# Kernel optimization log

Measured on AMD Instinct MI355X. Metric: run time of the kernel, lower is better.

The kernel has to match this reference:

```python
import jax, jax.numpy as jnp
import numpy as np

B, T, S = 64, 48, 48
E, H, L, V = 512, 1024, 2, 32000


def setup_inputs() -> dict:
    key = jax.random.key(0)
    ks = jax.random.split(key, 16)
    s = 0.02
    return {
        "tgt_input": jax.random.randint(ks[0], (B, T), 0, V),
        "h0": jax.random.normal(ks[1], (L, B, H), jnp.float32),
        "c0": jax.random.normal(ks[2], (L, B, H), jnp.float32),
        "encoder_output": jax.random.normal(ks[3], (B, S, H), jnp.float32),
        "src_key_padding_mask": jnp.zeros((B, S), bool),
        "embedding": jax.random.normal(ks[4], (V, E), jnp.float32) * s,
        "W_l": jax.random.normal(ks[5], (H, H), jnp.float32) * s,
        "b_l": jnp.zeros((H,), jnp.float32),
        "W_ih0": jax.random.normal(ks[6], (4 * H, E + H), jnp.float32) * s,
        "W_hh0": jax.random.normal(ks[7], (4 * H, H), jnp.float32) * s,
        "b_ih0": jnp.zeros((4 * H,), jnp.float32),
        "b_hh0": jnp.zeros((4 * H,), jnp.float32),
        "W_ih1": jax.random.normal(ks[8], (4 * H, H), jnp.float32) * s,
        "W_hh1": jax.random.normal(ks[9], (4 * H, H), jnp.float32) * s,
        "b_ih1": jnp.zeros((4 * H,), jnp.float32),
        "b_hh1": jnp.zeros((4 * H,), jnp.float32),
    }


def _lstm_cell(x, h, c, W_ih, W_hh, b_ih, b_hh):
    # PyTorch gate order: i, f, g, o
    gates = x @ W_ih.T + b_ih + h @ W_hh.T + b_hh  # [B, 4H]
    i, f, g, o = jnp.split(gates, 4, axis=-1)
    c_new = jax.nn.sigmoid(f) * c + jax.nn.sigmoid(i) * jnp.tanh(g)
    h_new = jax.nn.sigmoid(o) * jnp.tanh(c_new)
    return h_new, c_new


def reference(tgt_input, h0, c0, encoder_output, src_key_padding_mask,
              embedding, W_l, b_l,
              W_ih0, W_hh0, b_ih0, b_hh0,
              W_ih1, W_hh1, b_ih1, b_hh1):
    emb = embedding[tgt_input]              # [B, T, E]
    emb_t = jnp.transpose(emb, (1, 0, 2))   # [T, B, E]
    layers = ((W_ih0, W_hh0, b_ih0, b_hh0), (W_ih1, W_hh1, b_ih1, b_hh1))

    def step(carry, x_t):
        h, c = carry                        # [L, B, H] each
        # Luong attention with query = last-layer hidden state
        q = h[-1] @ W_l.T + b_l             # [B, H]
        scores = jnp.einsum('bh,bsh->bs', q, encoder_output)
        scores = jnp.where(src_key_padding_mask, -jnp.inf, scores)
        attn = jax.nn.softmax(scores, axis=-1)
        ctx = jnp.einsum('bs,bsh->bh', attn, encoder_output)  # [B, H]
        x = jnp.concatenate([x_t, ctx], axis=-1)              # [B, E+H]
        new_h, new_c = [], []
        for l, (W_ih, W_hh, b_ih, b_hh) in enumerate(layers):
            hn, cn = _lstm_cell(x, h[l], c[l], W_ih, W_hh, b_ih, b_hh)
            new_h.append(hn)
            new_c.append(cn)
            x = hn
        return (jnp.stack(new_h), jnp.stack(new_c)), x  # x = top-layer output

    (hn, cn), outs = jax.lax.scan(step, (h0, c0), emb_t)
    outputs = jnp.transpose(outs, (1, 0, 2))  # [B, T, H]
    return outputs, hn, cn
```

## Files before the change

kernel.cpp:

```cpp
#include <hip/hip_runtime.h>
#include <stdint.h>


using short8 = __attribute__((ext_vector_type(8))) short;
using f32x4  = __attribute__((ext_vector_type(4))) float;
typedef unsigned short u16;
typedef unsigned long long u64;

#define B_  64
#define T_  48
#define S_  48
#define H_  1024
#define E_  512

__device__ __forceinline__ float bf2f(u16 u) {
    union { unsigned int i; float f; } v; v.i = ((unsigned int)u) << 16; return v.f;
}
__device__ __forceinline__ u16 f2bf(float f) {
    union { float f; unsigned int i; } v; v.f = f;
    unsigned int r = v.i + 0x7fff + ((v.i >> 16) & 1);
    return (u16)(r >> 16);
}
__device__ __forceinline__ float sigm(float x) { return 1.f / (1.f + __expf(-x)); }


__global__ void cast_copy(u16* __restrict__ dst, int dld, int doff,
                          const float* __restrict__ src, int sld, int soff,
                          int rows, int colshift) {
    int cols = 1 << colshift;
    int total = rows << colshift;
    for (int i = blockIdx.x * blockDim.x + threadIdx.x; i < total;
         i += gridDim.x * blockDim.x) {
        int r = i >> colshift, c = i & (cols - 1);
        dst[(size_t)r * dld + doff + c] = f2bf(src[(size_t)r * sld + soff + c]);
    }
}

__global__ void transpose_cast(u16* __restrict__ dst, const float* __restrict__ src) {
    int idx = blockIdx.x * blockDim.x + threadIdx.x;
    int r = idx >> 10, c = idx & 1023;
    dst[idx] = f2bf(src[(size_t)c * 1024 + r]);
}

__global__ void embed_gather(u16* __restrict__ embA, const float* __restrict__ emb,
                             const int* __restrict__ tgt) {
    int row = blockIdx.x;
    int t = row >> 6, b = row & 63;
    int id = tgt[b * T_ + t];
    const float* s = emb + (size_t)id * E_;
    u16* d = embA + (size_t)row * E_;
    for (int e = threadIdx.x; e < E_; e += blockDim.x) d[e] = f2bf(s[e]);
}

__global__ void sbias_kernel(float* __restrict__ sbias, const float* __restrict__ enc,
                             const float* __restrict__ b_l) {
    int r = blockIdx.x, lane = threadIdx.x;
    const float* e = enc + (size_t)r * H_;
    float acc = 0.f;
    for (int k = lane; k < H_; k += 64) acc += b_l[k] * e[k];
    for (int o = 32; o; o >>= 1) acc += __shfl_xor(acc, o);
    if (lane == 0) sbias[r] = acc;
}

__global__ void init_state(u16* __restrict__ xa0_0, u16* __restrict__ xa1_0,
                           const float* __restrict__ h0) {
    int i = blockIdx.x * blockDim.x + threadIdx.x;
    int l = i >> 16, rem = i & 65535, b = rem >> 10, c = rem & 1023;
    u16 hb = f2bf(h0[i]);
    if (l == 0) xa0_0[b * 2048 + 1024 + c] = hb;
    else        xa1_0[b * 2048 + 1024 + c] = hb;
}

__global__ __launch_bounds__(256) void gemm64(
    const u16* __restrict__ A, const u16* __restrict__ W, u16* __restrict__ D,
    const float* __restrict__ bias1, const float* __restrict__ bias2,
    int N, int Kd)
{
    __shared__ float part[4][64][65];
    int tid = threadIdx.x, w = tid >> 6, lane = tid & 63;
    int hf = lane >> 4, q = lane & 15;
    int n0 = blockIdx.x * 64, m0 = blockIdx.y * 64;
    int ks = Kd >> 2;
    int kb = w * ks + hf * 8;
    const u16* ap = A + (size_t)(m0 + q) * Kd + kb;
    const u16* wp = W + (size_t)(n0 + q) * Kd + kb;
    f32x4 acc[4][4] = {};
    for (int k0 = 0; k0 < ks; k0 += 32) {
        short8 bf[4], af[4];
#pragma unroll
        for (int n = 0; n < 4; ++n) bf[n] = *(const short8*)(wp + (size_t)n * 16 * Kd + k0);
#pragma unroll
        for (int m = 0; m < 4; ++m) af[m] = *(const short8*)(ap + (size_t)m * 16 * Kd + k0);
#pragma unroll
        for (int m = 0; m < 4; ++m)
#pragma unroll
            for (int n = 0; n < 4; ++n)
                acc[m][n] = __builtin_amdgcn_mfma_f32_16x16x32_bf16(af[m], bf[n], acc[m][n], 0, 0, 0);
    }
#pragma unroll
    for (int m = 0; m < 4; ++m)
#pragma unroll
        for (int n = 0; n < 4; ++n)
#pragma unroll
            for (int r = 0; r < 4; ++r)
                part[w][m * 16 + hf * 4 + r][n * 16 + q] = acc[m][n][r];
    __syncthreads();
#pragma unroll
    for (int k = 0; k < 16; ++k) {
        int o = tid + k * 256;
        int row = o >> 6, col = o & 63;
        float v = part[0][row][col] + part[1][row][col]
                + part[2][row][col] + part[3][row][col];
        if (bias1) v += bias1[n0 + col] + bias2[n0 + col];
        D[(size_t)(m0 + row) * N + n0 + col] = f2bf(v);
    }
}


struct PParams {
    const float *W_ih0, *W_hh0, *W_ih1, *W_hh1;
    const u16  *preG, *encW, *encB;
    const float *sbias, *b_ih1, *b_hh1, *c0in;
    const unsigned char* mask;
    u16 *XA0, *XA1;
    float *out, *hn0, *hn1, *cn0, *cn1;
    unsigned *cnt;
};

__device__ __forceinline__ void gridarrive(unsigned* cnt, int ep, int g) {
    __syncthreads();
    if (threadIdx.x == 0)
        __hip_atomic_fetch_add(&cnt[g * 256 + ep], 1u,
                               __ATOMIC_RELAXED, __HIP_MEMORY_SCOPE_AGENT);
    asm volatile("" ::: "memory");
}
__device__ __forceinline__ void gridpoll(unsigned* cnt, int ep) {
    if (threadIdx.x < 64) {
        int spin = 0;
        for (;;) {
            unsigned v = __hip_atomic_load(&cnt[threadIdx.x * 256 + ep],
                                           __ATOMIC_RELAXED,
                                           __HIP_MEMORY_SCOPE_AGENT);
            if (__ballot(v >= 4u) == ~0ull) break;
            __builtin_amdgcn_s_sleep(2);
            if (++spin > (1 << 20)) break;
        }
    }
    asm volatile("" ::: "memory");
    __syncthreads();
}

__global__ void __launch_bounds__(256, 1) decoder_persistent(PParams P) {
    __shared__ u16 wlds[2][4096][8];
    __shared__ union {
        struct { float h1f[1056]; float sc[48][4]; float pr[48]; } at;
        float gates[64][20];
    } sm;

    const int tid = threadIdx.x, blk = blockIdx.x;
    const int w = tid >> 6, lane = tid & 63, g4 = lane >> 4, q = lane & 15;
    const int b2 = tid >> 2, j2 = tid & 3;
    const int colg = blk * 4 + j2;

    {
        int r = tid & 15, cb = tid >> 4;
        int grow = (r >> 2) * 1024 + blk * 4 + (r & 3);
#pragma unroll
        for (int l = 0; l < 2; ++l) {
            const float* Sa = l ? P.W_ih1 : P.W_ih0;
            const float* Sb = l ? P.W_hh1 : P.W_hh0;
            int sld  = l ? 1024 : 1536;
            int soff = l ? 0 : 512;
            for (int it = 0; it < 16; ++it) {
                int c = cb + it * 16;
                int k = c * 8;
                const float* src = (k < 1024)
                    ? (Sa + (size_t)grow * sld + soff + k)
                    : (Sb + (size_t)grow * 1024 + (k - 1024));
                float4 x0 = *(const float4*)(src);
                float4 x1 = *(const float4*)(src + 4);
                short8 v;
                v[0] = f2bf(x0.x); v[1] = f2bf(x0.y); v[2] = f2bf(x0.z); v[3] = f2bf(x0.w);
                v[4] = f2bf(x1.x); v[5] = f2bf(x1.y); v[6] = f2bf(x1.z); v[7] = f2bf(x1.w);
                *(short8*)&wlds[l][c * 16 + r][0] = v;
            }
        }
    }
    __syncthreads();
    float bsum[4];
#pragma unroll
    for (int g = 0; g < 4; ++g)
        bsum[g] = P.b_ih1[g * 1024 + colg] + P.b_hh1[g * 1024 + colg];
    float c0r = P.c0in[b2 * 1024 + colg];
    float c1r = P.c0in[65536 + b2 * 1024 + colg];

    const int ab = (blk & 7) * 8 + ((blk >> 3) & 7);
    const int aq = blk >> 6;
    int ep = 0;
    int t = 0;

    auto gemm_half = [&](const u16* Abase, int layer, int kbase, f32x4 seed) -> f32x4 {
        const u16* ap = Abase + (size_t)(w * 16 + q) * 2048 + kbase + g4 * 8;
        short8 xa[32];
#pragma unroll
        for (int kk = 0; kk < 32; ++kk)
            xa[kk] = *(const short8*)(ap + kk * 32);
        f32x4 a0 = seed, a1 = {}, a2 = {}, a3 = {};
        const int cbs = (kbase >> 3) + g4;
#pragma unroll
        for (int kk = 0; kk < 32; kk += 4) {
            a0 = __builtin_amdgcn_mfma_f32_16x16x32_bf16(
                xa[kk + 0], *(const short8*)&wlds[layer][(cbs + (kk + 0) * 4) * 16 + q][0], a0, 0, 0, 0);
            a1 = __builtin_amdgcn_mfma_f32_16x16x32_bf16(
                xa[kk + 1], *(const short8*)&wlds[layer][(cbs + (kk + 1) * 4) * 16 + q][0], a1, 0, 0, 0);
            a2 = __builtin_amdgcn_mfma_f32_16x16x32_bf16(
                xa[kk + 2], *(const short8*)&wlds[layer][(cbs + (kk + 2) * 4) * 16 + q][0], a2, 0, 0, 0);
            a3 = __builtin_amdgcn_mfma_f32_16x16x32_bf16(
                xa[kk + 3], *(const short8*)&wlds[layer][(cbs + (kk + 3) * 4) * 16 + q][0], a3, 0, 0, 0);
        }
        return (a0 + a1) + (a2 + a3);
    };

    auto lstm_phase = [&](const u16* Abase, int layer, f32x4 seed,
                          float add0, float add1, float add2, float add3,
                          float& creg, u16* dA, u16* dB, float* outp,
                          float* hnO, float* cnO, int doLast) {
        f32x4 g = gemm_half(Abase, layer, 0, seed);
#pragma unroll
        for (int r = 0; r < 4; ++r) sm.gates[w * 16 + g4 * 4 + r][q] = g[r];
        __syncthreads();
        float gi = sm.gates[b2][j2]      + add0;
        float gf = sm.gates[b2][4 + j2]  + add1;
        float gg = sm.gates[b2][8 + j2]  + add2;
        float go = sm.gates[b2][12 + j2] + add3;
        float cnew = sigm(gf) * creg + sigm(gi) * tanhf(gg);
        float hnew = sigm(go) * tanhf(cnew);
        creg = cnew;
        ((u16*)&sm.gates[b2][16])[j2] = f2bf(hnew);
        if (outp) outp[(size_t)(b2 * T_ + t) * H_ + colg] = hnew;
        if (doLast) { hnO[b2 * 1024 + colg] = hnew; cnO[b2 * 1024 + colg] = cnew; }
        __syncthreads();
        if (tid < 64) {
            u64 pk;
            __builtin_memcpy(&pk, (const u16*)&sm.gates[tid][16], 8);
            __hip_atomic_store((u64*)(dA + tid * 2048 + blk * 4), pk,
                               __ATOMIC_RELAXED, __HIP_MEMORY_SCOPE_AGENT);
            if (dB)
                __hip_atomic_store((u64*)(dB + tid * 2048 + blk * 4), pk,
                                   __ATOMIC_RELAXED, __HIP_MEMORY_SCOPE_AGENT);
        }
    };

    for (t = 0; t < T_; ++t) {
        const int last = (t == T_ - 1);
        u16* xa0c = P.XA0 + (size_t)t * 131072;
        u16* xa0n = P.XA0 + (size_t)(t + 1) * 131072;
        u16* xa1c = P.XA1 + (size_t)t * 131072;
        u16* xa1n = P.XA1 + (size_t)(t + 1) * 131072;

        for (int i = tid; i < H_; i += 256)
            sm.at.h1f[(i >> 8) * 264 + (i & 255)] = bf2f(xa1c[ab * 2048 + 1024 + i]);
        __syncthreads();
        if (tid < 192) {
            int s = tid >> 2, kq = tid & 3;
            const u16* ew = P.encW + ((size_t)ab * S_ + s) * H_ + kq * 256;
            const float2* hp = (const float2*)(sm.at.h1f + kq * 264);
            float p0 = 0.f, p1 = 0.f, p2 = 0.f, p3 = 0.f;
#pragma unroll
            for (int k = 0; k < 256; k += 32) {
                short8 v0 = *(const short8*)(ew + k);
                short8 v1 = *(const short8*)(ew + k + 8);
                short8 v2 = *(const short8*)(ew + k + 16);
                short8 v3 = *(const short8*)(ew + k + 24);
#pragma unroll
                for (int e = 0; e < 8; e += 2) {
                    float2 h0v = hp[(k >> 1) + (e >> 1)];
                    p0 += h0v.x * bf2f(((u16*)&v0)[e]) + h0v.y * bf2f(((u16*)&v0)[e + 1]);
                    float2 h1v = hp[(k >> 1) + 4 + (e >> 1)];
                    p1 += h1v.x * bf2f(((u16*)&v1)[e]) + h1v.y * bf2f(((u16*)&v1)[e + 1]);
                    float2 h2v = hp[(k >> 1) + 8 + (e >> 1)];
                    p2 += h2v.x * bf2f(((u16*)&v2)[e]) + h2v.y * bf2f(((u16*)&v2)[e + 1]);
                    float2 h3v = hp[(k >> 1) + 12 + (e >> 1)];
                    p3 += h3v.x * bf2f(((u16*)&v3)[e]) + h3v.y * bf2f(((u16*)&v3)[e + 1]);
                }
            }
            sm.at.sc[s][kq] = (p0 + p1) + (p2 + p3);
        }
        __syncthreads();
        if (tid < 64) {
            float v = -3.0e38f;
            if (tid < S_) {
                v = sm.at.sc[tid][0] + sm.at.sc[tid][1] + sm.at.sc[tid][2]
                  + sm.at.sc[tid][3] + P.sbias[ab * S_ + tid];
                if (P.mask[ab * S_ + tid]) v = -3.0e38f;
            }
            float mx = v;
            for (int o = 32; o; o >>= 1) mx = fmaxf(mx, __shfl_xor(mx, o));
            float e = (tid < S_) ? __expf(v - mx) : 0.f;
            float su = e;
            for (int o = 32; o; o >>= 1) su += __shfl_xor(su, o);
            if (tid < S_) sm.at.pr[tid] = e / su;
        }
        __syncthreads();
        {
            int col = aq * 256 + tid;
            const u16* eb = P.encB + (size_t)ab * S_ * H_ + col;
            float a0 = 0.f, a1 = 0.f, a2 = 0.f, a3 = 0.f;
#pragma unroll
            for (int s = 0; s < 48; s += 4) {
                a0 += sm.at.pr[s + 0] * bf2f(eb[(size_t)(s + 0) * H_]);
                a1 += sm.at.pr[s + 1] * bf2f(eb[(size_t)(s + 1) * H_]);
                a2 += sm.at.pr[s + 2] * bf2f(eb[(size_t)(s + 2) * H_]);
                a3 += sm.at.pr[s + 3] * bf2f(eb[(size_t)(s + 3) * H_]);
            }
            u16 myb = f2bf((a0 + a1) + (a2 + a3));
            int other = __shfl_xor((int)myb, 1);
            if ((tid & 1) == 0) {
                unsigned pk = (unsigned)myb | ((unsigned)(u16)other << 16);
                __hip_atomic_store((unsigned*)(xa0c + ab * 2048 + col), pk,
                                   __ATOMIC_RELAXED, __HIP_MEMORY_SCOPE_AGENT);
            }
        }
        const u16* pgp = P.preG + ((size_t)t * 64 + b2) * 4096 + colg;
        u16 pg0 = pgp[0], pg1 = pgp[1024], pg2 = pgp[2048], pg3 = pgp[3072];
        gridarrive(P.cnt, ++ep, ab);
        f32x4 g0p = gemm_half(xa0c, 0, 1024, f32x4{});
        f32x4 g1p = gemm_half(xa1c, 1, 1024, f32x4{});
        gridpoll(P.cnt, ep);

        lstm_phase(xa0c, 0, g0p, bf2f(pg0), bf2f(pg1), bf2f(pg2), bf2f(pg3),
                   c0r, xa1c, xa0n + 1024, nullptr, P.hn0, P.cn0, last);
        gridarrive(P.cnt, ++ep, ab);
        gridpoll(P.cnt, ep);

        lstm_phase(xa1c, 1, g1p, bsum[0], bsum[1], bsum[2], bsum[3],
                   c1r, xa1n + 1024, nullptr, P.out, P.hn1, P.cn1, last);
        gridarrive(P.cnt, ++ep, ab);
        gridpoll(P.cnt, ep);
    }
}


extern "C" void kernel_launch(void* const* d_in, const int* in_sizes, int n_in,
                              void* d_out, int out_size, void* d_ws, size_t ws_size,
                              hipStream_t stream) {
    const int*   tgt      = (const int*)d_in[0];
    const float* h0       = (const float*)d_in[1];
    const float* c0in     = (const float*)d_in[2];
    const float* enc      = (const float*)d_in[3];
    const unsigned char* mask = (const unsigned char*)d_in[4];
    const float* embedding= (const float*)d_in[5];
    const float* W_l      = (const float*)d_in[6];
    const float* b_l      = (const float*)d_in[7];
    const float* W_ih0    = (const float*)d_in[8];
    const float* W_hh0    = (const float*)d_in[9];
    const float* b_ih0    = (const float*)d_in[10];
    const float* b_hh0    = (const float*)d_in[11];
    const float* W_ih1    = (const float*)d_in[12];
    const float* W_hh1    = (const float*)d_in[13];
    const float* b_ih1    = (const float*)d_in[14];
    const float* b_hh1    = (const float*)d_in[15];
    float* out = (float*)d_out;

    char* ws = (char*)d_ws;
    u16* W0emb = (u16*)ws;               ws += (size_t)4096 * 512 * 2;
    u16* WlT   = (u16*)ws;               ws += (size_t)1024 * 1024 * 2;
    u16* embA  = (u16*)ws;               ws += (size_t)3072 * 512 * 2;
    u16* encB  = (u16*)ws;               ws += (size_t)3072 * 1024 * 2;
    u16* encWb = (u16*)ws;               ws += (size_t)3072 * 1024 * 2;
    float* sbias = (float*)ws;           ws += (size_t)3072 * 4;
    u16* preG  = (u16*)ws;               ws += (size_t)3072 * 4096 * 2;
    u16* XA0   = (u16*)ws;               ws += (size_t)49 * 131072 * 2;
    u16* XA1   = (u16*)ws;               ws += (size_t)49 * 131072 * 2;
    unsigned* bar = (unsigned*)ws;       ws += 262144;

    cast_copy<<<2048, 256, 0, stream>>>(W0emb, 512, 0, W_ih0, 1536, 0, 4096, 9);
    cast_copy<<<2048, 256, 0, stream>>>(encB, 1024, 0, enc, 1024, 0, 3072, 10);
    transpose_cast<<<4096, 256, 0, stream>>>(WlT, W_l);
    embed_gather<<<3072, 256, 0, stream>>>(embA, embedding, tgt);
    init_state<<<512, 256, 0, stream>>>(XA0, XA1, h0);
    sbias_kernel<<<3072, 64, 0, stream>>>(sbias, enc, b_l);
    gemm64<<<dim3(64, 48), 256, 0, stream>>>(embA, W0emb, preG, b_ih0, b_hh0, 4096, 512);
    gemm64<<<dim3(16, 48), 256, 0, stream>>>(encB, WlT, encWb, nullptr, nullptr, 1024, 1024);
    hipMemsetAsync(bar, 0, 262144, stream);

    PParams prm;
    prm.W_ih0 = W_ih0; prm.W_hh0 = W_hh0; prm.W_ih1 = W_ih1; prm.W_hh1 = W_hh1;
    prm.preG = preG; prm.encW = encWb; prm.encB = encB;
    prm.sbias = sbias; prm.b_ih1 = b_ih1; prm.b_hh1 = b_hh1; prm.c0in = c0in;
    prm.mask = mask;
    prm.XA0 = XA0; prm.XA1 = XA1;
    prm.out = out;
    prm.hn0 = out + 3145728; prm.hn1 = out + 3145728 + 65536;
    prm.cn0 = out + 3276800; prm.cn1 = out + 3276800 + 65536;
    prm.cnt = bar;
    decoder_persistent<<<256, 256, 0, stream>>>(prm);

    (void)in_sizes; (void)n_in; (void)out_size; (void)ws_size;
}
```

Baseline: 1.405 ms.

## Use master-block barrier with flags and overlap recurrent GEMM halves across phases

Grid barrier polling is centralised: block 0 polls all 64 group counters and publishes per-group release flags, so the other blocks spin on a single flag with one thread. The h-part GEMMs are rescheduled: layer-1 recurrent GEMM runs between layer-0 LSTM and its barrier, and the next step's layer-0 GEMM runs before the end-of-step barrier. This spreads matrix work into the barrier wait windows instead of doing both before the first barrier. It adds a hop through block 0 on every barrier, removes the sleep in polling, and relies on the state slices read by each GEMM being complete when the GEMM starts.

```diff
diff --git a/kernel.cpp b/kernel.cpp
--- a/kernel.cpp
+++ b/kernel.cpp
@@ -124,7 +124,7 @@
     const unsigned char* mask;
     u16 *XA0, *XA1;
     float *out, *hn0, *hn1, *cn0, *cn1;
-    unsigned *cnt;
+    unsigned *cnt, *flags;
 };
 
 __device__ __forceinline__ void gridarrive(unsigned* cnt, int ep, int g) {
@@ -134,15 +134,25 @@
                                __ATOMIC_RELAXED, __HIP_MEMORY_SCOPE_AGENT);
     asm volatile("" ::: "memory");
 }
-__device__ __forceinline__ void gridpoll(unsigned* cnt, int ep) {
-    if (threadIdx.x < 64) {
+__device__ __forceinline__ void gridpoll(unsigned* cnt, unsigned* flags,
+                                         int ep, int g) {
+    if (blockIdx.x == 0) {
+        if (threadIdx.x < 64) {
+            int spin = 0;
+            for (;;) {
+                unsigned v = __hip_atomic_load(&cnt[threadIdx.x * 256 + ep],
+                                               __ATOMIC_RELAXED,
+                                               __HIP_MEMORY_SCOPE_AGENT);
+                if (__ballot(v >= 4u) == ~0ull) break;
+                if (++spin > (1 << 20)) break;
+            }
+            __hip_atomic_store(&flags[threadIdx.x * 256 + ep], 1u,
+                               __ATOMIC_RELAXED, __HIP_MEMORY_SCOPE_AGENT);
+        }
+    } else if (threadIdx.x == 0) {
         int spin = 0;
-        for (;;) {
-            unsigned v = __hip_atomic_load(&cnt[threadIdx.x * 256 + ep],
-                                           __ATOMIC_RELAXED,
-                                           __HIP_MEMORY_SCOPE_AGENT);
-            if (__ballot(v >= 4u) == ~0ull) break;
-            __builtin_amdgcn_s_sleep(2);
+        while (!__hip_atomic_load(&flags[g * 256 + ep], __ATOMIC_RELAXED,
+                                  __HIP_MEMORY_SCOPE_AGENT)) {
             if (++spin > (1 << 20)) break;
         }
     }
@@ -251,6 +261,9 @@
         }
     };
 
+    f32x4 g0p = gemm_half(P.XA0, 0, 1024, f32x4{});
+    f32x4 g1p = {};
+
     for (t = 0; t < T_; ++t) {
         const int last = (t == T_ - 1);
         u16* xa0c = P.XA0 + (size_t)t * 131072;
@@ -321,22 +334,22 @@
                                    __ATOMIC_RELAXED, __HIP_MEMORY_SCOPE_AGENT);
             }
         }
+        gridarrive(P.cnt, ++ep, ab);
         const u16* pgp = P.preG + ((size_t)t * 64 + b2) * 4096 + colg;
         u16 pg0 = pgp[0], pg1 = pgp[1024], pg2 = pgp[2048], pg3 = pgp[3072];
-        gridarrive(P.cnt, ++ep, ab);
-        f32x4 g0p = gemm_half(xa0c, 0, 1024, f32x4{});
-        f32x4 g1p = gemm_half(xa1c, 1, 1024, f32x4{});
-        gridpoll(P.cnt, ep);
+        gridpoll(P.cnt, P.flags, ep, ab);
 
         lstm_phase(xa0c, 0, g0p, bf2f(pg0), bf2f(pg1), bf2f(pg2), bf2f(pg3),
                    c0r, xa1c, xa0n + 1024, nullptr, P.hn0, P.cn0, last);
         gridarrive(P.cnt, ++ep, ab);
-        gridpoll(P.cnt, ep);
+        g1p = gemm_half(xa1c, 1, 1024, f32x4{});
+        gridpoll(P.cnt, P.flags, ep, ab);
 
         lstm_phase(xa1c, 1, g1p, bsum[0], bsum[1], bsum[2], bsum[3],
                    c1r, xa1n + 1024, nullptr, P.out, P.hn1, P.cn1, last);
         gridarrive(P.cnt, ++ep, ab);
-        gridpoll(P.cnt, ep);
+        g0p = gemm_half(xa0n, 0, 1024, f32x4{});
+        gridpoll(P.cnt, P.flags, ep, ab);
     }
 }
 
@@ -393,7 +406,7 @@
     prm.out = out;
     prm.hn0 = out + 3145728; prm.hn1 = out + 3145728 + 65536;
     prm.cn0 = out + 3276800; prm.cn1 = out + 3276800 + 65536;
-    prm.cnt = bar;
+    prm.cnt = bar; prm.flags = bar + 16384;
     decoder_persistent<<<256, 256, 0, stream>>>(prm);
 
     (void)in_sizes; (void)n_in; (void)out_size; (void)ws_size;
```

Result: faster. 1.322 ms, median of 2 (-5.9%).
